# Performance work log

Hardware: AMD Instinct MI355X
Metric: run time of the kernel (lower is better)

## Reference

```python
import jax, jax.numpy as jnp
import numpy as np

D_MODEL = 1024
NUM_HEADS = 16
DEPTH = D_MODEL // NUM_HEADS


def setup_inputs() -> dict:
    key = jax.random.key(0)
    ks = jax.random.split(key, 11)
    B, S = 2, 2048
    s = 1.0 / np.sqrt(D_MODEL)
    return {
        "q": jax.random.normal(ks[0], (B, S, D_MODEL), jnp.float32),
        "k": jax.random.normal(ks[1], (B, S, D_MODEL), jnp.float32),
        "v": jax.random.normal(ks[2], (B, S, D_MODEL), jnp.float32),
        "wq": jax.random.normal(ks[3], (D_MODEL, D_MODEL), jnp.float32) * s,
        "bq": jax.random.normal(ks[4], (D_MODEL,), jnp.float32) * s,
        "wk": jax.random.normal(ks[5], (D_MODEL, D_MODEL), jnp.float32) * s,
        "bk": jax.random.normal(ks[6], (D_MODEL,), jnp.float32) * s,
        "wv": jax.random.normal(ks[7], (D_MODEL, D_MODEL), jnp.float32) * s,
        "bv": jax.random.normal(ks[8], (D_MODEL,), jnp.float32) * s,
        "wo": jax.random.normal(ks[9], (D_MODEL, D_MODEL), jnp.float32) * s,
        "bo": jax.random.normal(ks[10], (D_MODEL,), jnp.float32) * s,
    }


def _split_heads(x, B):
    # [B, S, D] -> [B, H, S, depth]
    return x.reshape(B, -1, NUM_HEADS, DEPTH).transpose(0, 2, 1, 3)


def reference(q, k, v, wq, bq, wk, bk, wv, bv, wo, bo):
    B, S, _ = q.shape
    # torch Linear: y = x @ W.T + b
    qh = _split_heads(q @ wq.T + bq, B)
    kh = _split_heads(k @ wk.T + bk, B)
    vh = _split_heads(v @ wv.T + bv, B)
    scale = jnp.sqrt(jnp.asarray(DEPTH, jnp.float32))
    scores = jnp.einsum("bhqd,bhkd->bhqk", qh, kh) / scale  # [B,H,S,S]
    attn = jax.nn.softmax(scores, axis=-1)
    out = jnp.einsum("bhqk,bhkd->bhqd", attn, vh)
    out = out.transpose(0, 2, 1, 3).reshape(B, S, D_MODEL)
    return out @ wo.T + bo
```

## Files before the change

kernel.cpp:

```cpp
#include <hip/hip_runtime.h>
#include <hip/hip_bf16.h>
#include <math.h>

#define D_MODEL 1024
#define NUM_HEADS 16
#define DEPTH 64
#define BATCH 2
#define SEQ 2048
#define N_TOK (BATCH * SEQ)

typedef short bf16x8 __attribute__((ext_vector_type(8)));
typedef _Float16 f16x8 __attribute__((ext_vector_type(8)));
typedef float f32x4  __attribute__((ext_vector_type(4)));
typedef unsigned short u16x8 __attribute__((ext_vector_type(8)));
typedef unsigned short u16x4 __attribute__((ext_vector_type(4)));
typedef unsigned int u32x4 __attribute__((ext_vector_type(4)));

__device__ __forceinline__ unsigned short f2b(float x) {
    return __builtin_bit_cast(unsigned short, __float2bfloat16(x));
}
__device__ __forceinline__ float b2f(unsigned short h) {
    return __builtin_bit_cast(float, (unsigned int)h << 16);
}
__device__ __forceinline__ unsigned short f2h(float x) {
    return __builtin_bit_cast(unsigned short, (_Float16)x);
}
__device__ __forceinline__ float h2f(unsigned short h) {
    return (float)__builtin_bit_cast(_Float16, h);
}

__device__ __forceinline__ void pl32_swap(unsigned int& x, unsigned int& y) {
    auto r = __builtin_amdgcn_permlane32_swap(x, y, false, false);
    x = (unsigned int)r[0]; y = (unsigned int)r[1];
}
__device__ __forceinline__ void pl16_swap(unsigned int& x, unsigned int& y) {
    auto r = __builtin_amdgcn_permlane16_swap(x, y, false, false);
    x = (unsigned int)r[0]; y = (unsigned int)r[1];
}

__global__ __launch_bounds__(256) void prep_weights(
    const float* __restrict__ s0, const float* __restrict__ s1,
    const float* __restrict__ s2, const float* __restrict__ s3,
    unsigned short* __restrict__ f0, unsigned short* __restrict__ f1,
    unsigned short* __restrict__ f2, unsigned short* __restrict__ f3,
    int n8)
{
    const int i = blockIdx.x * 256 + threadIdx.x;
    if (i >= n8) return;
    const int which = blockIdx.y;
    const float* src = (which == 0) ? s0 : (which == 1) ? s1 : (which == 2) ? s2 : s3;
    unsigned short* dst = (which == 0) ? f0 : (which == 1) ? f1 : (which == 2) ? f2 : f3;
    const float4 a0 = ((const float4*)src)[2 * i];
    const float4 a1 = ((const float4*)src)[2 * i + 1];
    const float xs[8] = {a0.x, a0.y, a0.z, a0.w, a1.x, a1.y, a1.z, a1.w};
    u16x8 o;
    #pragma unroll
    for (int e = 0; e < 8; ++e) o[e] = f2h(xs[e]);
    *(u16x8*)&dst[(size_t)i * 8] = o;
}

__global__ __launch_bounds__(256, 3) void qkv_gemm(
    const float* __restrict__ Aq, const float* __restrict__ Ak,
    const float* __restrict__ Av,
    const unsigned short* __restrict__ Wq, const unsigned short* __restrict__ Wk,
    const unsigned short* __restrict__ Wv,
    const float* __restrict__ bq, const float* __restrict__ bk,
    const float* __restrict__ bv,
    void* __restrict__ Yq, void* __restrict__ Yk, void* __restrict__ Yvp)
{
    __shared__ unsigned short sA[128][64];
    __shared__ unsigned short sB[2][128][64];

    const int flat = (blockIdx.z * 32 + blockIdx.y) * 8 + blockIdx.x;
    const int swz  = (flat & 7) * 96 + (flat >> 3);
    const int bx = swz & 7;
    const int by = (swz >> 3) & 31;
    const int bz = swz >> 8;

    const float* Af = (bz == 0) ? Aq : (bz == 1) ? Ak : Av;
    const unsigned short* Bf = (bz == 0) ? Wq : (bz == 1) ? Wk : Wv;
    const float* bias = (bz == 0) ? bq : (bz == 1) ? bk : bv;
    const float scale = (bz == 0) ? 0.125f : 1.0f;
    const int mode = (bz == 2) ? 2 : 1;
    void* Yv = (bz == 0) ? Yq : (bz == 1) ? Yk : Yvp;

    const int tid  = threadIdx.x;
    const int wave = tid >> 6;
    const int lane = tid & 63;
    const int quad = lane >> 4;
    const int l16  = lane & 15;
    const int wm   = wave >> 1;
    const int wn   = wave & 1;

    const int j0 = bx * 128;
    const int i0 = by * 128;

    const int sc  = tid & 7;
    const int r32 = tid >> 3;

    f32x4 acc[4][4] = {};

    float4 fq[4][2];

    auto loadA = [&](int s) {
        const int k0 = s * 64;
        #pragma unroll
        for (int p = 0; p < 4; ++p) {
            const int row = p * 32 + r32;
            const int cg = (sc ^ (row & 7)) * 8;
            const float* srcp = &Af[(size_t)(i0 + row) * 1024 + k0 + cg];
            fq[p][0] = *(const float4*)srcp;
            fq[p][1] = *(const float4*)(srcp + 4);
        }
    };
    auto writeA = [&]() {
        #pragma unroll
        for (int p = 0; p < 4; ++p) {
            const int row = p * 32 + r32;
            const float xs[8] = {fq[p][0].x, fq[p][0].y, fq[p][0].z, fq[p][0].w,
                                 fq[p][1].x, fq[p][1].y, fq[p][1].z, fq[p][1].w};
            u16x8 o;
            #pragma unroll
            for (int e = 0; e < 8; ++e) o[e] = f2h(xs[e]);
            *(u16x8*)&sA[row][sc * 8] = o;
        }
    };
    auto stageB = [&](int buf, int s) {
        const int k0 = s * 64;
        #pragma unroll
        for (int p = 0; p < 4; ++p) {
            const int row = p * 32 + r32;
            const int cg = (sc ^ (row & 7)) * 8;
            __builtin_amdgcn_global_load_lds(
                (const __attribute__((address_space(1))) unsigned int*)
                    &Bf[(size_t)(j0 + row) * 1024 + k0 + cg],
                (__attribute__((address_space(3))) unsigned int*)&sB[buf][row][sc * 8],
                16, 0, 0);
        }
    };

    loadA(0);
    stageB(0, 0);
    writeA();
    __asm__ volatile("s_waitcnt vmcnt(0)" ::: "memory");
    __syncthreads();

    int cur = 0;
    for (int s = 0; s < 16; ++s) {
        if (s + 1 < 16) { loadA(s + 1); stageB(cur ^ 1, s + 1); }

        #pragma unroll
        for (int ks = 0; ks < 2; ++ks) {
            f16x8 a[4], b[4];
            #pragma unroll
            for (int mt = 0; mt < 4; ++mt) {
                const int row = wm * 64 + mt * 16 + l16;
                const int c = (((ks * 4 + quad) ^ (row & 7))) * 8;
                a[mt] = *(const f16x8*)&sA[row][c];
            }
            #pragma unroll
            for (int nt = 0; nt < 4; ++nt) {
                const int row = wn * 64 + nt * 16 + l16;
                const int c = (((ks * 4 + quad) ^ (row & 7))) * 8;
                b[nt] = *(const f16x8*)&sB[cur][row][c];
            }
            #pragma unroll
            for (int mt = 0; mt < 4; ++mt)
                #pragma unroll
                for (int nt = 0; nt < 4; ++nt)
                    acc[mt][nt] = __builtin_amdgcn_mfma_f32_16x16x32_f16(a[mt], b[nt], acc[mt][nt], 0, 0, 0);
        }

        __syncthreads();
        if (s + 1 < 16) {
            writeA();
            __asm__ volatile("s_waitcnt vmcnt(0)" ::: "memory");
        }
        __syncthreads();
        cur ^= 1;
    }

    float bvv[4];
    #pragma unroll
    for (int nt = 0; nt < 4; ++nt)
        bvv[nt] = bias[j0 + wn * 64 + nt * 16 + l16];

    #pragma unroll
    for (int mt = 0; mt < 4; ++mt) {
        const int ibase = i0 + wm * 64 + mt * 16 + quad * 4;
        #pragma unroll
        for (int nt = 0; nt < 4; ++nt) {
            const int j = j0 + wn * 64 + nt * 16 + l16;
            const int h = j >> 6, d = j & 63;
            if (mode == 1) {
                __hip_bfloat16* Y = (__hip_bfloat16*)Yv;
                #pragma unroll
                for (int r = 0; r < 4; ++r) {
                    const int i = ibase + r;
                    const int b = i >> 11, ss = i & (SEQ - 1);
                    Y[(((size_t)(b * NUM_HEADS + h) * SEQ) + ss) * DEPTH + d] =
                        __float2bfloat16((acc[mt][nt][r] + bvv[nt]) * scale);
                }
            } else {
                unsigned short* Y = (unsigned short*)Yv;
                const int b = ibase >> 11;
                u16x4 pack;
                #pragma unroll
                for (int r = 0; r < 4; ++r)
                    pack[r] = f2b((acc[mt][nt][r] + bvv[nt]) * scale);
                *(u16x4*)&Y[(((size_t)(b * NUM_HEADS + h) * DEPTH) + d) * SEQ
                            + (ibase & (SEQ - 1))] = pack;
            }
        }
    }
}

__global__ __launch_bounds__(512, 2) void gemm_f16x2(
    const unsigned short* __restrict__ Ahi,
    const unsigned short* __restrict__ Alo,
    const unsigned short* __restrict__ Bf,
    const float* __restrict__ bias,
    float* __restrict__ Y,
    float scale)
{
    __shared__ unsigned short sAh[128][64];
    __shared__ unsigned short sAl[128][64];
    __shared__ unsigned short sB [128][64];

    const int tid  = threadIdx.x;
    const int wave = tid >> 6;
    const int lane = tid & 63;
    const int quad = lane >> 4;
    const int l16  = lane & 15;
    const int wm   = wave >> 1;
    const int wn   = wave & 1;

    const int j0 = blockIdx.x * 128;
    const int i0 = blockIdx.y * 128;

    const int sc  = tid & 7;
    const int r64 = tid >> 3;

    u16x8 preH[4], preL[2];

    auto prefetch = [&](int s) {
        const int k0 = s * 64;
        #pragma unroll
        for (int p = 0; p < 4; ++p) {
            const int row256 = p * 64 + r64;
            const bool isA = row256 < 128;
            const int row = isA ? row256 : row256 - 128;
            const int grow = (isA ? i0 : j0) + row;
            const int cg = (sc ^ (row & 7)) * 8;
            const size_t go = (size_t)grow * 1024 + k0 + cg;
            if (isA) {
                preH[p] = *(const u16x8*)&Ahi[go];
                preL[p] = *(const u16x8*)&Alo[go];
            } else {
                preH[p] = *(const u16x8*)&Bf[go];
            }
        }
    };

    prefetch(0);

    f32x4 acc[2][4] = {};

    for (int s = 0; s < 16; ++s) {
        __syncthreads();

        #pragma unroll
        for (int p = 0; p < 4; ++p) {
            const int row256 = p * 64 + r64;
            const bool isA = row256 < 128;
            const int row = isA ? row256 : row256 - 128;
            if (isA) {
                *(u16x8*)&sAh[row][sc * 8] = preH[p];
                *(u16x8*)&sAl[row][sc * 8] = preL[p];
            } else {
                *(u16x8*)&sB[row][sc * 8] = preH[p];
            }
        }
        __syncthreads();

        if (s + 1 < 16) prefetch(s + 1);

        #pragma unroll
        for (int ks = 0; ks < 2; ++ks) {
            f16x8 ah[2], al[2], b[4];
            #pragma unroll
            for (int mt = 0; mt < 2; ++mt) {
                const int row = wm * 32 + mt * 16 + l16;
                const int c = (((ks * 4 + quad) ^ (row & 7))) * 8;
                ah[mt] = *(const f16x8*)&sAh[row][c];
                al[mt] = *(const f16x8*)&sAl[row][c];
            }
            #pragma unroll
            for (int nt = 0; nt < 4; ++nt) {
                const int row = wn * 64 + nt * 16 + l16;
                const int c = (((ks * 4 + quad) ^ (row & 7))) * 8;
                b[nt] = *(const f16x8*)&sB[row][c];
            }
            #pragma unroll
            for (int mt = 0; mt < 2; ++mt)
                #pragma unroll
                for (int nt = 0; nt < 4; ++nt) {
                    acc[mt][nt] = __builtin_amdgcn_mfma_f32_16x16x32_f16(ah[mt], b[nt], acc[mt][nt], 0, 0, 0);
                    acc[mt][nt] = __builtin_amdgcn_mfma_f32_16x16x32_f16(al[mt], b[nt], acc[mt][nt], 0, 0, 0);
                }
        }
    }

    float bv[4];
    #pragma unroll
    for (int nt = 0; nt < 4; ++nt)
        bv[nt] = bias[j0 + wn * 64 + nt * 16 + l16];

    #pragma unroll
    for (int mt = 0; mt < 2; ++mt) {
        const int ibase = i0 + wm * 32 + mt * 16 + quad * 4;
        #pragma unroll
        for (int nt = 0; nt < 4; ++nt) {
            const int j = j0 + wn * 64 + nt * 16 + l16;
            #pragma unroll
            for (int r = 0; r < 4; ++r)
                Y[(size_t)(ibase + r) * 1024 + j] = (acc[mt][nt][r] + bv[nt]) * scale;
        }
    }
}

__global__ __launch_bounds__(256, 2) void flash_attn_mfma(
    const __hip_bfloat16* __restrict__ Qg,
    const __hip_bfloat16* __restrict__ Kg,
    const __hip_bfloat16* __restrict__ Vg,
    unsigned short* __restrict__ OHi,
    unsigned short* __restrict__ OLo)
{
    __shared__ unsigned short Ks[64][72];
    __shared__ unsigned short Vt[64][72];

    const int tid  = threadIdx.x;
    const int wave = tid >> 6;
    const int lane = tid & 63;
    const int quad = lane >> 4;
    const int l16  = lane & 15;

    const int flat = blockIdx.x;
    const int swz  = (flat & 7) * 64 + (flat >> 3);
    const int bh = swz >> 4;
    const int q0 = (swz & 15) * 128;

    const unsigned short* Qu = (const unsigned short*)Qg + (size_t)bh * SEQ * DEPTH;
    const unsigned short* Ku = (const unsigned short*)Kg + (size_t)bh * SEQ * DEPTH;
    const unsigned short* Vu = (const unsigned short*)Vg + (size_t)bh * DEPTH * SEQ;

    const int qrowA = q0 + wave * 16 + l16;
    const int qrowB = qrowA + 64;
    bf16x8 qfA[2], qfB[2];
    qfA[0] = *(const bf16x8*)&Qu[(size_t)qrowA * DEPTH + quad * 8];
    qfA[1] = *(const bf16x8*)&Qu[(size_t)qrowA * DEPTH + 32 + quad * 8];
    qfB[0] = *(const bf16x8*)&Qu[(size_t)qrowB * DEPTH + quad * 8];
    qfB[1] = *(const bf16x8*)&Qu[(size_t)qrowB * DEPTH + 32 + quad * 8];

    bf16x8 ones;
    #pragma unroll
    for (int e = 0; e < 8; ++e) ones[e] = (short)0x3F80;

    f32x4 o_accA[4] = {}, o_accB[4] = {};
    f32x4 l_accA = {0.f, 0.f, 0.f, 0.f};
    f32x4 l_accB = {0.f, 0.f, 0.f, 0.f};

    const int srow = tid >> 3;
    const int sc8  = (tid & 7) * 8;
    u16x8 kpre[2], vpre[2];
    #pragma unroll
    for (int it = 0; it < 2; ++it) {
        const int row = it * 32 + srow;
        kpre[it] = *(const u16x8*)&Ku[(size_t)row * DEPTH + sc8];
        vpre[it] = *(const u16x8*)&Vu[(size_t)row * SEQ + sc8];
    }

    auto make_pf = [&](const f32x4 s[4], bf16x8 pf[2]) {
        unsigned int Wp[4][2];
        #pragma unroll
        for (int nt = 0; nt < 4; ++nt) {
            #pragma unroll
            for (int b = 0; b < 2; ++b) {
                const unsigned int lo = f2b(__expf(s[nt][2 * b]));
                const unsigned int hi = f2b(__expf(s[nt][2 * b + 1]));
                Wp[nt][b] = lo | (hi << 16);
            }
        }
        unsigned int pw[8];
        #pragma unroll
        for (int b = 0; b < 2; ++b) {
            unsigned int x = Wp[0][b], y = Wp[1][b];
            pl32_swap(x, y);
            pl16_swap(x, y);
            pw[b] = x; pw[2 + b] = y;
            x = Wp[2][b]; y = Wp[3][b];
            pl32_swap(x, y);
            pl16_swap(x, y);
            pw[4 + b] = x; pw[6 + b] = y;
        }
        u32x4 t0, t1;
        #pragma unroll
        for (int j = 0; j < 4; ++j) { t0[j] = pw[j]; t1[j] = pw[4 + j]; }
        pf[0] = __builtin_bit_cast(bf16x8, t0);
        pf[1] = __builtin_bit_cast(bf16x8, t1);
    };

    for (int t = 0; t < 32; ++t) {
        __syncthreads();

        #pragma unroll
        for (int it = 0; it < 2; ++it) {
            const int row = it * 32 + srow;
            *(u16x8*)&Ks[row][sc8] = kpre[it];
            *(u16x8*)&Vt[row][sc8] = vpre[it];
        }
        __syncthreads();

        if (t + 1 < 32) {
            const int k0 = (t + 1) * 64;
            #pragma unroll
            for (int it = 0; it < 2; ++it) {
                const int row = it * 32 + srow;
                kpre[it] = *(const u16x8*)&Ku[(size_t)(k0 + row) * DEPTH + sc8];
                vpre[it] = *(const u16x8*)&Vu[(size_t)row * SEQ + k0 + sc8];
            }
        }

        f32x4 sA[4], sB[4];
        #pragma unroll
        for (int nt = 0; nt < 4; ++nt) {
            sA[nt] = f32x4{0.f, 0.f, 0.f, 0.f};
            sB[nt] = f32x4{0.f, 0.f, 0.f, 0.f};
            bf16x8 kf0 = *(const bf16x8*)&Ks[nt * 16 + l16][quad * 8];
            sA[nt] = __builtin_amdgcn_mfma_f32_16x16x32_bf16(kf0, qfA[0], sA[nt], 0, 0, 0);
            sB[nt] = __builtin_amdgcn_mfma_f32_16x16x32_bf16(kf0, qfB[0], sB[nt], 0, 0, 0);
            bf16x8 kf1 = *(const bf16x8*)&Ks[nt * 16 + l16][32 + quad * 8];
            sA[nt] = __builtin_amdgcn_mfma_f32_16x16x32_bf16(kf1, qfA[1], sA[nt], 0, 0, 0);
            sB[nt] = __builtin_amdgcn_mfma_f32_16x16x32_bf16(kf1, qfB[1], sB[nt], 0, 0, 0);
        }

        bf16x8 pfA[2], pfB[2];
        make_pf(sA, pfA);
        make_pf(sB, pfB);

        #pragma unroll
        for (int nt = 0; nt < 4; ++nt) {
            bf16x8 vf0 = *(const bf16x8*)&Vt[nt * 16 + l16][quad * 8];
            o_accA[nt] = __builtin_amdgcn_mfma_f32_16x16x32_bf16(pfA[0], vf0, o_accA[nt], 0, 0, 0);
            o_accB[nt] = __builtin_amdgcn_mfma_f32_16x16x32_bf16(pfB[0], vf0, o_accB[nt], 0, 0, 0);
            bf16x8 vf1 = *(const bf16x8*)&Vt[nt * 16 + l16][32 + quad * 8];
            o_accA[nt] = __builtin_amdgcn_mfma_f32_16x16x32_bf16(pfA[1], vf1, o_accA[nt], 0, 0, 0);
            o_accB[nt] = __builtin_amdgcn_mfma_f32_16x16x32_bf16(pfB[1], vf1, o_accB[nt], 0, 0, 0);
        }
        l_accA = __builtin_amdgcn_mfma_f32_16x16x32_bf16(pfA[0], ones, l_accA, 0, 0, 0);
        l_accA = __builtin_amdgcn_mfma_f32_16x16x32_bf16(pfA[1], ones, l_accA, 0, 0, 0);
        l_accB = __builtin_amdgcn_mfma_f32_16x16x32_bf16(pfB[0], ones, l_accB, 0, 0, 0);
        l_accB = __builtin_amdgcn_mfma_f32_16x16x32_bf16(pfB[1], ones, l_accB, 0, 0, 0);
    }

    const int b = bh / NUM_HEADS;
    const int h = bh % NUM_HEADS;
    #pragma unroll
    for (int r = 0; r < 4; ++r) {
        const float invA = 1.f / l_accA[r];
        const float invB = 1.f / l_accB[r];
        const int rowA = q0 + wave * 16 + quad * 4 + r;
        const int rowB = rowA + 64;
        #pragma unroll
        for (int nt = 0; nt < 4; ++nt) {
            {
                const float o = o_accA[nt][r] * invA;
                const size_t idx = ((size_t)(b * SEQ + rowA)) * D_MODEL + h * DEPTH + nt * 16 + l16;
                const unsigned short hbits = f2h(o);
                OHi[idx] = hbits;
                OLo[idx] = f2h(o - h2f(hbits));
            }
            {
                const float o = o_accB[nt][r] * invB;
                const size_t idx = ((size_t)(b * SEQ + rowB)) * D_MODEL + h * DEPTH + nt * 16 + l16;
                const unsigned short hbits = f2h(o);
                OHi[idx] = hbits;
                OLo[idx] = f2h(o - h2f(hbits));
            }
        }
    }
}

extern "C" void kernel_launch(void* const* d_in, const int* in_sizes, int n_in,
                              void* d_out, int out_size, void* d_ws, size_t ws_size,
                              hipStream_t stream) {
    const float* q  = (const float*)d_in[0];
    const float* k  = (const float*)d_in[1];
    const float* v  = (const float*)d_in[2];
    const float* wq = (const float*)d_in[3];
    const float* bq = (const float*)d_in[4];
    const float* wk = (const float*)d_in[5];
    const float* bk = (const float*)d_in[6];
    const float* wv = (const float*)d_in[7];
    const float* bv = (const float*)d_in[8];
    const float* wo = (const float*)d_in[9];
    const float* bo = (const float*)d_in[10];
    float* out = (float*)d_out;

    char* ws = (char*)d_ws;
    const size_t MB = 1024 * 1024;
    unsigned short* AoHi = (unsigned short*)(ws);
    unsigned short* AoLo = (unsigned short*)(ws + 8 * MB);
    unsigned short* WqF  = (unsigned short*)(ws + 16 * MB);
    unsigned short* WkF  = (unsigned short*)(ws + 18 * MB);
    unsigned short* WvF  = (unsigned short*)(ws + 20 * MB);
    unsigned short* WoF  = (unsigned short*)(ws + 22 * MB);
    __hip_bfloat16* Qh   = (__hip_bfloat16*)(ws + 26 * MB);
    __hip_bfloat16* Kh   = (__hip_bfloat16*)(ws + 34 * MB);
    __hip_bfloat16* Vh   = (__hip_bfloat16*)(ws + 42 * MB);

    const int nW8 = D_MODEL * D_MODEL / 8;
    dim3 sb(256);

    prep_weights<<<dim3(nW8 / 256, 4), sb, 0, stream>>>(
        wq, wk, wv, wo, WqF, WkF, WvF, WoF, nW8);

    dim3 fblk(256);
    dim3 fgrid(D_MODEL / 128, N_TOK / 128, 3);
    qkv_gemm<<<fgrid, fblk, 0, stream>>>(
        q, k, v, WqF, WkF, WvF, bq, bk, bv, Qh, Kh, (void*)Vh);

    dim3 ablk(256);
    dim3 agrid(BATCH * NUM_HEADS * (SEQ / 128));
    flash_attn_mfma<<<agrid, ablk, 0, stream>>>(Qh, Kh, Vh, AoHi, AoLo);

    dim3 oblk(512);
    dim3 ogrid(D_MODEL / 128, N_TOK / 128);
    gemm_f16x2<<<ogrid, oblk, 0, stream>>>(AoHi, AoLo, WoF, bo, out, 1.0f);
}
```

Baseline: 233.3 us.

## Double-buffer K/V tiles via direct global-to-LDS loads with XOR swizzle

Replaces the register-staged K/V prefetch in the flash attention loop with direct global_load_lds transfers into a double-buffered shared-memory tile. This removes one barrier per iteration and the LDS store step. Padding is replaced by an XOR swizzle of 16-byte column groups to avoid bank conflicts. The risk is that the wait on outstanding loads now sits at the end of each iteration, and the swizzle and direct-load mapping must match exactly.

```diff
diff --git a/kernel.cpp b/kernel.cpp
--- a/kernel.cpp
+++ b/kernel.cpp
@@ -336,8 +336,8 @@
     unsigned short* __restrict__ OHi,
     unsigned short* __restrict__ OLo)
 {
-    __shared__ unsigned short Ks[64][72];
-    __shared__ unsigned short Vt[64][72];
+    __shared__ unsigned short Ks[2][64][64];
+    __shared__ unsigned short Vt[2][64][64];
 
     const int tid  = threadIdx.x;
     const int wave = tid >> 6;
@@ -370,15 +370,28 @@
     f32x4 l_accA = {0.f, 0.f, 0.f, 0.f};
     f32x4 l_accB = {0.f, 0.f, 0.f, 0.f};
 
-    const int srow = tid >> 3;
-    const int sc8  = (tid & 7) * 8;
-    u16x8 kpre[2], vpre[2];
-    #pragma unroll
-    for (int it = 0; it < 2; ++it) {
-        const int row = it * 32 + srow;
-        kpre[it] = *(const u16x8*)&Ku[(size_t)row * DEPTH + sc8];
-        vpre[it] = *(const u16x8*)&Vu[(size_t)row * SEQ + sc8];
-    }
+    const int lr8 = lane >> 3;
+    const int sc  = lane & 7;
+
+    auto stage = [&](int buf, int t) {
+        const int k0 = t * 64;
+        #pragma unroll
+        for (int it = 0; it < 2; ++it) {
+            const int rbase = it * 32 + wave * 8;
+            const int row = rbase + lr8;
+            const int cg = (sc ^ (row & 7)) * 8;
+            __builtin_amdgcn_global_load_lds(
+                (const __attribute__((address_space(1))) unsigned int*)
+                    &Ku[(size_t)(k0 + row) * DEPTH + cg],
+                (__attribute__((address_space(3))) unsigned int*)&Ks[buf][row][sc * 8],
+                16, 0, 0);
+            __builtin_amdgcn_global_load_lds(
+                (const __attribute__((address_space(1))) unsigned int*)
+                    &Vu[(size_t)row * SEQ + k0 + cg],
+                (__attribute__((address_space(3))) unsigned int*)&Vt[buf][row][sc * 8],
+                16, 0, 0);
+        }
+    };
 
     auto make_pf = [&](const f32x4 s[4], bf16x8 pf[2]) {
         unsigned int Wp[4][2];
@@ -410,36 +423,24 @@
         pf[1] = __builtin_bit_cast(bf16x8, t1);
     };
 
+    stage(0, 0);
+    __asm__ volatile("s_waitcnt vmcnt(0)" ::: "memory");
+    __syncthreads();
+
+    int cur = 0;
     for (int t = 0; t < 32; ++t) {
-        __syncthreads();
-
-        #pragma unroll
-        for (int it = 0; it < 2; ++it) {
-            const int row = it * 32 + srow;
-            *(u16x8*)&Ks[row][sc8] = kpre[it];
-            *(u16x8*)&Vt[row][sc8] = vpre[it];
-        }
-        __syncthreads();
-
-        if (t + 1 < 32) {
-            const int k0 = (t + 1) * 64;
-            #pragma unroll
-            for (int it = 0; it < 2; ++it) {
-                const int row = it * 32 + srow;
-                kpre[it] = *(const u16x8*)&Ku[(size_t)(k0 + row) * DEPTH + sc8];
-                vpre[it] = *(const u16x8*)&Vu[(size_t)row * SEQ + k0 + sc8];
-            }
-        }
+        if (t + 1 < 32) stage(cur ^ 1, t + 1);
 
         f32x4 sA[4], sB[4];
         #pragma unroll
         for (int nt = 0; nt < 4; ++nt) {
             sA[nt] = f32x4{0.f, 0.f, 0.f, 0.f};
             sB[nt] = f32x4{0.f, 0.f, 0.f, 0.f};
-            bf16x8 kf0 = *(const bf16x8*)&Ks[nt * 16 + l16][quad * 8];
+            const int row = nt * 16 + l16;
+            bf16x8 kf0 = *(const bf16x8*)&Ks[cur][row][((quad ^ (row & 7))) * 8];
             sA[nt] = __builtin_amdgcn_mfma_f32_16x16x32_bf16(kf0, qfA[0], sA[nt], 0, 0, 0);
             sB[nt] = __builtin_amdgcn_mfma_f32_16x16x32_bf16(kf0, qfB[0], sB[nt], 0, 0, 0);
-            bf16x8 kf1 = *(const bf16x8*)&Ks[nt * 16 + l16][32 + quad * 8];
+            bf16x8 kf1 = *(const bf16x8*)&Ks[cur][row][(((4 + quad) ^ (row & 7))) * 8];
             sA[nt] = __builtin_amdgcn_mfma_f32_16x16x32_bf16(kf1, qfA[1], sA[nt], 0, 0, 0);
             sB[nt] = __builtin_amdgcn_mfma_f32_16x16x32_bf16(kf1, qfB[1], sB[nt], 0, 0, 0);
         }
@@ -450,10 +451,11 @@
 
         #pragma unroll
         for (int nt = 0; nt < 4; ++nt) {
-            bf16x8 vf0 = *(const bf16x8*)&Vt[nt * 16 + l16][quad * 8];
+            const int row = nt * 16 + l16;
+            bf16x8 vf0 = *(const bf16x8*)&Vt[cur][row][((quad ^ (row & 7))) * 8];
             o_accA[nt] = __builtin_amdgcn_mfma_f32_16x16x32_bf16(pfA[0], vf0, o_accA[nt], 0, 0, 0);
             o_accB[nt] = __builtin_amdgcn_mfma_f32_16x16x32_bf16(pfB[0], vf0, o_accB[nt], 0, 0, 0);
-            bf16x8 vf1 = *(const bf16x8*)&Vt[nt * 16 + l16][32 + quad * 8];
+            bf16x8 vf1 = *(const bf16x8*)&Vt[cur][row][(((4 + quad) ^ (row & 7))) * 8];
             o_accA[nt] = __builtin_amdgcn_mfma_f32_16x16x32_bf16(pfA[1], vf1, o_accA[nt], 0, 0, 0);
             o_accB[nt] = __builtin_amdgcn_mfma_f32_16x16x32_bf16(pfB[1], vf1, o_accB[nt], 0, 0, 0);
         }
@@ -461,6 +463,12 @@
         l_accA = __builtin_amdgcn_mfma_f32_16x16x32_bf16(pfA[1], ones, l_accA, 0, 0, 0);
         l_accB = __builtin_amdgcn_mfma_f32_16x16x32_bf16(pfB[0], ones, l_accB, 0, 0, 0);
         l_accB = __builtin_amdgcn_mfma_f32_16x16x32_bf16(pfB[1], ones, l_accB, 0, 0, 0);
+
+        if (t + 1 < 32) {
+            __asm__ volatile("s_waitcnt vmcnt(0)" ::: "memory");
+            __syncthreads();
+        }
+        cur ^= 1;
     }
 
     const int b = bh / NUM_HEADS;
```

After: 242.2 us. 1.04x slower.
